# Kernel optimization log

Hardware: AMD Instinct MI355X
Metric: run time of the kernel (lower is better)

## Reference

```python
import jax, jax.numpy as jnp
import numpy as np

D = 768
H = 12
DH = D // H
DFF = 3072
EPS = 1e-5


def setup_inputs() -> dict:
    key = jax.random.key(0)
    ks = jax.random.split(key, 12)
    s = 0.02
    return {
        "x": jax.random.normal(ks[0], (1, 4096, D), jnp.float32),
        "wq": jax.random.normal(ks[1], (D, D), jnp.float32) * s,
        "wk": jax.random.normal(ks[2], (D, D), jnp.float32) * s,
        "wv": jax.random.normal(ks[3], (D, D), jnp.float32) * s,
        "wo": jax.random.normal(ks[4], (D, D), jnp.float32) * s,
        "bo": jnp.zeros((D,), jnp.float32),
        "gamma1": jnp.ones((D,), jnp.float32),
        "beta1": jnp.zeros((D,), jnp.float32),
        "gamma2": jnp.ones((D,), jnp.float32),
        "beta2": jnp.zeros((D,), jnp.float32),
        "w1": jax.random.normal(ks[5], (DFF, D), jnp.float32) * s,
        "b1": jnp.zeros((DFF,), jnp.float32),
        "w2": jax.random.normal(ks[6], (D, DFF), jnp.float32) * s,
        "b2": jnp.zeros((D,), jnp.float32),
    }


def layer_norm(x, gamma, beta):
    mean = jnp.mean(x, axis=-1, keepdims=True)
    var = jnp.mean((x - mean) ** 2, axis=-1, keepdims=True)  # biased variance
    return gamma * (x - mean) / jnp.sqrt(var + EPS) + beta


def reference(x, wq, wk, wv, wo, bo, gamma1, beta1, gamma2, beta2, w1, b1, w2, b2):
    B, T, _ = x.shape
    # --- pre-norm self-attention ---
    h = layer_norm(x, gamma1, beta1)
    q = (h @ wq.T).reshape(B, T, H, DH).transpose(0, 2, 1, 3)  # (B,H,T,dh)
    k = (h @ wk.T).reshape(B, T, H, DH).transpose(0, 2, 1, 3)
    v = (h @ wv.T).reshape(B, T, H, DH).transpose(0, 2, 1, 3)
    scores = jnp.einsum("bhqd,bhkd->bhqk", q, k) / np.sqrt(DH).astype(np.float32)
    probs = jax.nn.softmax(scores, axis=-1)  # dropout = identity (eval)
    attn = jnp.einsum("bhqk,bhkd->bhqd", probs, v)
    attn = attn.transpose(0, 2, 1, 3).reshape(B, T, D)
    x = x + attn @ wo.T + bo
    # --- pre-norm FFN ---
    h2 = layer_norm(x, gamma2, beta2)
    ff = jax.nn.gelu(h2 @ w1.T + b1, approximate=False) @ w2.T + b2
    return x + ff
```

## Files before the change

### kernel.cpp

```cpp
#include <hip/hip_runtime.h>
#include <hip/hip_bf16.h>
#include <math.h>

#define D_MODEL 768
#define NHEAD   12
#define DHEAD   64
#define DFF     3072
#define SEQ     4096

typedef __attribute__((ext_vector_type(8))) short bf16x8;
typedef __attribute__((ext_vector_type(4))) float f32x4;
typedef __attribute__((ext_vector_type(4))) unsigned int u32x4;

__device__ __forceinline__ unsigned short f2bf(float f) {
  union { float f; unsigned int i; } c; c.f = f;
  unsigned int r = c.i + 0x7fffu + ((c.i >> 16) & 1u);
  return (unsigned short)(r >> 16);
}
__device__ __forceinline__ unsigned int pack_bf2(float a, float b) {
  __hip_bfloat162 h = __float22bfloat162_rn(make_float2(a, b));
  return *reinterpret_cast<unsigned int*>(&h);
}
__device__ __forceinline__ float exp2_hw(float x) {
  float r;
  asm("v_exp_f32 %0, %1" : "=v"(r) : "v"(x));
  return r;
}

__global__ void cvt_all(const float* __restrict__ wq, const float* __restrict__ wk,
                        const float* __restrict__ wv, const float* __restrict__ wo,
                        const float* __restrict__ w1, const float* __restrict__ w2,
                        unsigned short* __restrict__ out) {
  const int N4 = 7077888 / 4;
  int i4 = blockIdx.x * blockDim.x + threadIdx.x;
  int stride = gridDim.x * blockDim.x;
  for (; i4 < N4; i4 += stride) {
    int i = i4 * 4;
    const float* src; int j;
    if (i < 2359296) {
      int a = i / 589824; j = i - a * 589824;
      src = a == 0 ? wq : a == 1 ? wk : a == 2 ? wv : wo;
    } else if (i < 4718592) { src = w1; j = i - 2359296; }
    else                    { src = w2; j = i - 4718592; }
    float4 f = *(const float4*)(src + j);
    ushort4 o4;
    o4.x = f2bf(f.x); o4.y = f2bf(f.y); o4.z = f2bf(f.z); o4.w = f2bf(f.w);
    *(ushort4*)(out + i) = o4;
  }
}

__global__ __launch_bounds__(256) void ln_kernel(const float* __restrict__ x,
                                                 const float* __restrict__ gamma,
                                                 const float* __restrict__ beta,
                                                 unsigned short* __restrict__ out) {
  int row = blockIdx.x, tid = threadIdx.x;
  int lane = tid & 63, wv = tid >> 6;
  const float* xr = x + (size_t)row * D_MODEL;
  float v0 = xr[tid], v1 = xr[tid + 256], v2 = xr[tid + 512];
  float s = v0 + v1 + v2;
  __shared__ float red[4];
#pragma unroll
  for (int off = 32; off; off >>= 1) s += __shfl_down(s, off);
  if (lane == 0) red[wv] = s;
  __syncthreads();
  float mean = (red[0] + red[1] + red[2] + red[3]) * (1.0f / D_MODEL);
  __syncthreads();
  float d0 = v0 - mean, d1 = v1 - mean, d2 = v2 - mean;
  float sq = d0 * d0 + d1 * d1 + d2 * d2;
#pragma unroll
  for (int off = 32; off; off >>= 1) sq += __shfl_xor(sq, off);
  if (lane == 0) red[wv] = sq;
  __syncthreads();
  float var = (red[0] + red[1] + red[2] + red[3]) * (1.0f / D_MODEL);
  float rstd = rsqrtf(var + 1e-5f);
  unsigned short* orow = out + (size_t)row * D_MODEL;
  orow[tid]       = f2bf(gamma[tid]       * d0 * rstd + beta[tid]);
  orow[tid + 256] = f2bf(gamma[tid + 256] * d1 * rstd + beta[tid + 256]);
  orow[tid + 512] = f2bf(gamma[tid + 512] * d2 * rstd + beta[tid + 512]);
}

__device__ __forceinline__ void gld_lds(const void* g, void* l) {
  __builtin_amdgcn_global_load_lds((const __attribute__((address_space(1))) unsigned int*)g,
                                   (__attribute__((address_space(3))) unsigned int*)l, 16, 0, 0);
}

template <int MODE, int WM>
__global__ __launch_bounds__(256) void gemm_bt(const unsigned short* __restrict__ A,
                                               const unsigned short* __restrict__ B,
                                               int M, int N, int K,
                                               const float* __restrict__ bias,
                                               const float* __restrict__ residual,
                                               void* __restrict__ out) {
  const int MR = WM / 16;
  const int ASZ = 2 * WM * 32;
  __shared__ __align__(16) unsigned short As[2 * 128 * 32];
  __shared__ __align__(16) unsigned short Bs[2 * 128 * 32];
  const int tid = threadIdx.x;
  const int lane = tid & 63;
  const int wv = tid >> 6;
  const int lo = lane & 15, hi = lane >> 4;
  const int wr = wv >> 1, wc = wv & 1;
  const int row0 = blockIdx.x * (2 * WM), col0 = blockIdx.y * 128;
  const int srow = tid >> 2, scol = (tid & 3) * 8;

  f32x4 zero = {0.f, 0.f, 0.f, 0.f};
  f32x4 acc[MR][4];
#pragma unroll
  for (int m = 0; m < MR; ++m)
#pragma unroll
    for (int n = 0; n < 4; ++n) acc[m][n] = zero;

  const unsigned short* Abase = A + (size_t)(row0 + srow) * K + scol;
  const unsigned short* Bbase = B + (size_t)(col0 + srow) * K + scol;

  auto STAGE = [&](int bi, int kt) {
    unsigned short* Ad = As + bi * ASZ;
    unsigned short* Bd = Bs + bi * 4096;
    gld_lds(Abase + kt, Ad + tid * 8);
    if (WM == 64) gld_lds(Abase + kt + (size_t)64 * K, Ad + 2048 + tid * 8);
    gld_lds(Bbase + kt,                  Bd + tid * 8);
    gld_lds(Bbase + kt + (size_t)64 * K, Bd + 2048 + tid * 8);
  };

  int buf = 0;
  STAGE(0, 0);
  for (int kt = 0; kt < K; kt += 32) {
    __syncthreads();
    if (kt + 32 < K) STAGE(buf ^ 1, kt + 32);
    const unsigned short* Ab = As + buf * ASZ;
    const unsigned short* Bb = Bs + buf * 4096;
    bf16x8 a[MR], b[4];
#pragma unroll
    for (int m = 0; m < MR; ++m)
      a[m] = *(const bf16x8*)(Ab + (wr * WM + m * 16 + lo) * 32 + hi * 8);
#pragma unroll
    for (int n = 0; n < 4; ++n)
      b[n] = *(const bf16x8*)(Bb + (wc * 64 + n * 16 + lo) * 32 + hi * 8);
#pragma unroll
    for (int m = 0; m < MR; ++m)
#pragma unroll
      for (int n = 0; n < 4; ++n)
        acc[m][n] = __builtin_amdgcn_mfma_f32_16x16x32_bf16(a[m], b[n], acc[m][n], 0, 0, 0);
    buf ^= 1;
  }

#pragma unroll
  for (int m = 0; m < MR; ++m) {
#pragma unroll
    for (int n = 0; n < 4; ++n) {
#pragma unroll
      for (int r = 0; r < 4; ++r) {
        int row = row0 + wr * WM + m * 16 + hi * 4 + r;
        int col = col0 + wc * 64 + n * 16 + lo;
        float v = acc[m][n][r];
        if (MODE == 2) {
          ((float*)out)[(size_t)row * N + col] = v + bias[col] + residual[(size_t)row * N + col];
        } else if (MODE == 3) {
          float t = v + bias[col];
          float g = t * __builtin_amdgcn_rcpf(1.0f + __expf(-1.702f * t));
          ((unsigned short*)out)[(size_t)row * N + col] = f2bf(g);
        } else {
          int seg = col / 768;
          int c = col - seg * 768;
          unsigned short* ob = (unsigned short*)out + (size_t)seg * SEQ * D_MODEL;
          float vv = (seg == 0) ? v * 0.18033688011112042f : v;
          if (seg < 2) ob[((size_t)(c >> 6) * M + row) * 64 + (c & 63)] = f2bf(vv);
          else         ob[(size_t)c * M + row] = f2bf(vv);
        }
      }
    }
  }
}

__global__ __launch_bounds__(256, 4) void attn_kernel(const unsigned short* __restrict__ qb,
                                                      const unsigned short* __restrict__ kb,
                                                      const unsigned short* __restrict__ vt,
                                                      unsigned short* __restrict__ outb) {
  __shared__ __align__(16) unsigned short lds[16384 + 128];
  const int tid = threadIdx.x;
  const int lane = tid & 63, wv = tid >> 6;
  const int lo = lane & 15, hi = lane >> 4;
  const int b = blockIdx.x;
  const int u = (b & 7) * 96 + (b >> 3);
  const int head = u >> 6;
  const int q0 = (u & 63) * 64;
  const unsigned short* qh = qb + (size_t)head * SEQ * 64;
  const unsigned short* kh = kb + (size_t)head * SEQ * 64;
  const unsigned short* vh = vt + (size_t)head * 64 * SEQ;

  const int rho  = tid >> 3;
  const int r3   = rho & 7;
  const int krow = (rho & 35) | ((rho & 16) >> 2) | ((rho & 12) << 1);
  const int kofs = krow * 64 + ((tid & 7) ^ r3) * 8;
  const int vcol = ((tid & 7) ^ r3) * 8;
  const int sw   = (lo & 7) << 3;

  f32x4 zero = {0.f, 0.f, 0.f, 0.f};
  bf16x8 qf[2];
#pragma unroll
  for (int kk = 0; kk < 2; ++kk)
    qf[kk] = *(const bf16x8*)(qh + (size_t)(q0 + wv * 16 + lo) * 64 + kk * 32 + hi * 8);

  f32x4 o[4];
  float li = 0.f;
#pragma unroll
  for (int n = 0; n < 4; ++n) o[n] = zero;

  auto STAGE = [&](int bi, int kt) {
    unsigned short* Kd = lds + bi * 4096;
    unsigned short* Vd = lds + 8192 + bi * 4096;
    const unsigned short* kp = kh + (size_t)kt * 64;
    gld_lds(kp + kofs,        Kd + tid * 8);
    gld_lds(kp + 2048 + kofs, Kd + 2048 + tid * 8);
    const unsigned short* vp = vh + kt + vcol;
    gld_lds(vp + (size_t)rho * SEQ,        Vd + tid * 8);
    gld_lds(vp + (size_t)(32 + rho) * SEQ, Vd + 2048 + tid * 8);
  };

  int buf = 0;
  STAGE(0, 0);
  __syncthreads();
  for (int kt = 0; kt < SEQ; kt += 64) {
    if (kt + 64 < SEQ) STAGE(buf ^ 1, kt + 64);
    const unsigned short* Kb = lds + buf * 4096;
    const unsigned short* Vb = lds + 8192 + buf * 4096;
    f32x4 s[4];
    __builtin_amdgcn_s_setprio(1);
#pragma unroll
    for (int n = 0; n < 4; ++n) {
      const int ra = (n * 16 + lo) * 64;
      bf16x8 k0 = *(const bf16x8*)(Kb + ((ra + hi * 8) ^ sw));
      bf16x8 k1 = *(const bf16x8*)(Kb + ((ra + 32 + hi * 8) ^ sw));
      f32x4 t = __builtin_amdgcn_mfma_f32_16x16x32_bf16(k0, qf[0], zero, 0, 0, 0);
      s[n]    = __builtin_amdgcn_mfma_f32_16x16x32_bf16(k1, qf[1], t, 0, 0, 0);
    }
    __builtin_amdgcn_s_setprio(0);
    unsigned int p2[4][2];
#pragma unroll
    for (int n = 0; n < 4; ++n) {
      float e0 = exp2_hw(s[n][0]);
      float e1 = exp2_hw(s[n][1]);
      float e2 = exp2_hw(s[n][2]);
      float e3 = exp2_hw(s[n][3]);
      li += (e0 + e1) + (e2 + e3);
      p2[n][0] = pack_bf2(e0, e1);
      p2[n][1] = pack_bf2(e2, e3);
    }
    __builtin_amdgcn_s_setprio(1);
#pragma unroll
    for (int c = 0; c < 2; ++c) {
      u32x4 pu;
      pu[0] = p2[2 * c][0]; pu[1] = p2[2 * c][1];
      pu[2] = p2[2 * c + 1][0]; pu[3] = p2[2 * c + 1][1];
      bf16x8 pf = *(bf16x8*)&pu;
#pragma unroll
      for (int n = 0; n < 4; ++n) {
        bf16x8 vf = *(const bf16x8*)(Vb + (((n * 16 + lo) * 64 + c * 32 + hi * 8) ^ sw));
        o[n] = __builtin_amdgcn_mfma_f32_16x16x32_bf16(pf, vf, o[n], 0, 0, 0);
      }
    }
    __builtin_amdgcn_s_setprio(0);
    __syncthreads();
    buf ^= 1;
  }

  {
    float t = li;
    t += __shfl_xor(t, 16);
    t += __shfl_xor(t, 32);
    float* pL = (float*)(lds + 16384);
    if (lane < 16) pL[wv * 16 + lane] = 1.0f / t;
  }
  float inv[4];
  {
    float* pL = (float*)(lds + 16384);
#pragma unroll
    for (int r = 0; r < 4; ++r) inv[r] = pL[wv * 16 + hi * 4 + r];
  }

  __syncthreads();
  float* Ow = (float*)lds + wv * 1088;
#pragma unroll
  for (int n = 0; n < 4; ++n)
#pragma unroll
    for (int r = 0; r < 4; ++r)
      Ow[(hi * 4 + r) * 68 + n * 16 + lo] = o[n][r] * inv[r];
  {
    int row = lane >> 2, c0 = (lane & 3) * 16;
    unsigned short tmp[16];
#pragma unroll
    for (int i = 0; i < 16; ++i) tmp[i] = f2bf(Ow[row * 68 + c0 + i]);
    unsigned short* dst = outb + (size_t)(q0 + wv * 16 + row) * D_MODEL + head * 64 + c0;
    *(bf16x8*)dst       = *(const bf16x8*)tmp;
    *(bf16x8*)(dst + 8) = *(const bf16x8*)(tmp + 8);
  }
}

extern "C" void kernel_launch(void* const* d_in, const int* in_sizes, int n_in,
                              void* d_out, int out_size, void* d_ws, size_t ws_size,
                              hipStream_t stream) {
  const float* x      = (const float*)d_in[0];
  const float* wq     = (const float*)d_in[1];
  const float* wk     = (const float*)d_in[2];
  const float* wv     = (const float*)d_in[3];
  const float* wo     = (const float*)d_in[4];
  const float* bo     = (const float*)d_in[5];
  const float* gamma1 = (const float*)d_in[6];
  const float* beta1  = (const float*)d_in[7];
  const float* gamma2 = (const float*)d_in[8];
  const float* beta2  = (const float*)d_in[9];
  const float* w1     = (const float*)d_in[10];
  const float* b1     = (const float*)d_in[11];
  const float* w2     = (const float*)d_in[12];
  const float* b2     = (const float*)d_in[13];
  float* out = (float*)d_out;

  char* ws = (char*)d_ws;
  size_t off = 0;
  auto alloc = [&](size_t bytes) -> void* {
    void* p = ws + off;
    off += (bytes + 255) & ~(size_t)255;
    return p;
  };
  unsigned short* wq_b = (unsigned short*)alloc((size_t)D_MODEL * D_MODEL * 2);
  unsigned short* wk_b = (unsigned short*)alloc((size_t)D_MODEL * D_MODEL * 2);
  unsigned short* wv_b = (unsigned short*)alloc((size_t)D_MODEL * D_MODEL * 2);
  unsigned short* wo_b = (unsigned short*)alloc((size_t)D_MODEL * D_MODEL * 2);
  unsigned short* w1_b = (unsigned short*)alloc((size_t)DFF * D_MODEL * 2);
  unsigned short* w2_b = (unsigned short*)alloc((size_t)D_MODEL * DFF * 2);
  unsigned short* h1   = (unsigned short*)alloc((size_t)SEQ * D_MODEL * 2);
  unsigned short* qh   = (unsigned short*)alloc((size_t)SEQ * D_MODEL * 2);
  unsigned short* kh   = (unsigned short*)alloc((size_t)SEQ * D_MODEL * 2);
  unsigned short* vth  = (unsigned short*)alloc((size_t)SEQ * D_MODEL * 2);
  unsigned short* attnb= (unsigned short*)alloc((size_t)SEQ * D_MODEL * 2);
  float*          x2   = (float*)alloc((size_t)SEQ * D_MODEL * 4);
  unsigned short* h2   = (unsigned short*)alloc((size_t)SEQ * D_MODEL * 2);
  unsigned short* ffb  = (unsigned short*)alloc((size_t)SEQ * DFF * 2);
  (void)ws_size; (void)in_sizes; (void)n_in; (void)out_size;

  cvt_all<<<2048, 256, 0, stream>>>(wq, wk, wv, wo, w1, w2, wq_b);

  ln_kernel<<<SEQ, 256, 0, stream>>>(x, gamma1, beta1, h1);

  dim3 gqkv(SEQ / 128, 2304 / 128);
  gemm_bt<4, 64><<<gqkv, 256, 0, stream>>>(h1, wq_b, SEQ, 2304, D_MODEL, nullptr, nullptr, qh);

  attn_kernel<<<NHEAD * (SEQ / 64), 256, 0, stream>>>(qh, kh, vth, attnb);

  dim3 gwo(SEQ / 64, D_MODEL / 128);
  gemm_bt<2, 32><<<gwo, 256, 0, stream>>>(attnb, wo_b, SEQ, D_MODEL, D_MODEL, bo, x, x2);

  ln_kernel<<<SEQ, 256, 0, stream>>>(x2, gamma2, beta2, h2);

  dim3 gf1(SEQ / 128, DFF / 128);
  gemm_bt<3, 64><<<gf1, 256, 0, stream>>>(h2, w1_b, SEQ, DFF, D_MODEL, b1, nullptr, ffb);

  dim3 gf2(SEQ / 64, D_MODEL / 128);
  gemm_bt<2, 32><<<gf2, 256, 0, stream>>>(ffb, w2_b, SEQ, D_MODEL, DFF, b2, x2, out);
}
```

Measured before the change: 215.2 us.

## Split attention KV range across wave pairs and give each wave two query tiles

Each block's four waves now form two pairs. Each pair processes half of the key/value sequence in its own LDS region, and each wave computes 32 query rows (two M-tiles), so every K/V fragment loaded from LDS feeds two MFMAs. Partial outputs and row sums from the two halves are combined through LDS before normalisation and the bf16 store. The aim is fewer LDS reads per MFMA and a shorter serial KV loop. In exchange, LDS use doubles, launch bounds drop to 2 blocks per CU, and register pressure rises.

```diff
diff --git a/kernel.cpp b/kernel.cpp
--- a/kernel.cpp
+++ b/kernel.cpp
@@ -172,14 +172,16 @@
   }
 }
 
-__global__ __launch_bounds__(256, 4) void attn_kernel(const unsigned short* __restrict__ qb,
+__global__ __launch_bounds__(256, 2) void attn_kernel(const unsigned short* __restrict__ qb,
                                                       const unsigned short* __restrict__ kb,
                                                       const unsigned short* __restrict__ vt,
                                                       unsigned short* __restrict__ outb) {
-  __shared__ __align__(16) unsigned short lds[16384 + 128];
+  __shared__ __align__(16) unsigned short lds[32768];
   const int tid = threadIdx.x;
   const int lane = tid & 63, wv = tid >> 6;
   const int lo = lane & 15, hi = lane >> 4;
+  const int st = wv >> 1;
+  const int qm = wv & 1;
   const int b = blockIdx.x;
   const int u = (b & 7) * 96 + (b >> 3);
   const int head = u >> 6;
@@ -188,75 +190,92 @@
   const unsigned short* kh = kb + (size_t)head * SEQ * 64;
   const unsigned short* vh = vt + (size_t)head * 64 * SEQ;
 
-  const int rho  = tid >> 3;
-  const int r3   = rho & 7;
-  const int krow = (rho & 35) | ((rho & 16) >> 2) | ((rho & 12) << 1);
-  const int kofs = krow * 64 + ((tid & 7) ^ r3) * 8;
-  const int vcol = ((tid & 7) ^ r3) * 8;
-  const int sw   = (lo & 7) << 3;
+  const int ts   = tid >> 7;
+  const int t7   = tid & 127;
+  const int trow = t7 >> 3, tc8 = t7 & 7;
+  const int csw  = (tc8 ^ (trow & 7)) * 8;
+  int kofs[4], vofs[4];
+#pragma unroll
+  for (int o = 0; o < 4; ++o) {
+    int rho = o * 16 + trow;
+    int r5 = rho & 31, half = rho >> 5;
+    int pk = (r5 & 3) | ((r5 & 16) >> 2) | ((r5 & 12) << 1);
+    kofs[o] = (half * 32 + pk) * 64 + csw;
+    vofs[o] = rho * SEQ + csw;
+  }
+  const int sw = (lo & 7) << 3;
 
   f32x4 zero = {0.f, 0.f, 0.f, 0.f};
-  bf16x8 qf[2];
-#pragma unroll
-  for (int kk = 0; kk < 2; ++kk)
-    qf[kk] = *(const bf16x8*)(qh + (size_t)(q0 + wv * 16 + lo) * 64 + kk * 32 + hi * 8);
-
-  f32x4 o[4];
-  float li = 0.f;
-#pragma unroll
-  for (int n = 0; n < 4; ++n) o[n] = zero;
+  bf16x8 qf[2][2];
+#pragma unroll
+  for (int m = 0; m < 2; ++m)
+#pragma unroll
+    for (int kk = 0; kk < 2; ++kk)
+      qf[m][kk] = *(const bf16x8*)(qh + (size_t)(q0 + qm * 32 + m * 16 + lo) * 64 + kk * 32 + hi * 8);
+
+  f32x4 o[2][4];
+  float li[2] = {0.f, 0.f};
+#pragma unroll
+  for (int m = 0; m < 2; ++m)
+#pragma unroll
+    for (int n = 0; n < 4; ++n) o[m][n] = zero;
 
   auto STAGE = [&](int bi, int kt) {
-    unsigned short* Kd = lds + bi * 4096;
-    unsigned short* Vd = lds + 8192 + bi * 4096;
-    const unsigned short* kp = kh + (size_t)kt * 64;
-    gld_lds(kp + kofs,        Kd + tid * 8);
-    gld_lds(kp + 2048 + kofs, Kd + 2048 + tid * 8);
-    const unsigned short* vp = vh + kt + vcol;
-    gld_lds(vp + (size_t)rho * SEQ,        Vd + tid * 8);
-    gld_lds(vp + (size_t)(32 + rho) * SEQ, Vd + 2048 + tid * 8);
+    unsigned short* Kd = lds + ts * 16384 + bi * 4096;
+    unsigned short* Vd = lds + ts * 16384 + 8192 + bi * 4096;
+    const unsigned short* kp = kh + (size_t)(ts * 2048 + kt) * 64;
+    const unsigned short* vp = vh + ts * 2048 + kt;
+#pragma unroll
+    for (int oo = 0; oo < 4; ++oo) {
+      gld_lds(kp + kofs[oo], Kd + oo * 1024 + t7 * 8);
+      gld_lds(vp + vofs[oo], Vd + oo * 1024 + t7 * 8);
+    }
   };
 
+  const unsigned short* base = lds + st * 16384;
   int buf = 0;
   STAGE(0, 0);
   __syncthreads();
-  for (int kt = 0; kt < SEQ; kt += 64) {
-    if (kt + 64 < SEQ) STAGE(buf ^ 1, kt + 64);
-    const unsigned short* Kb = lds + buf * 4096;
-    const unsigned short* Vb = lds + 8192 + buf * 4096;
-    f32x4 s[4];
-    __builtin_amdgcn_s_setprio(1);
+  for (int kt = 0; kt < 2048; kt += 64) {
+    if (kt + 64 < 2048) STAGE(buf ^ 1, kt + 64);
+    const unsigned short* Kb = base + buf * 4096;
+    const unsigned short* Vb = base + 8192 + buf * 4096;
+    unsigned int p2[2][4][2];
 #pragma unroll
     for (int n = 0; n < 4; ++n) {
       const int ra = (n * 16 + lo) * 64;
       bf16x8 k0 = *(const bf16x8*)(Kb + ((ra + hi * 8) ^ sw));
       bf16x8 k1 = *(const bf16x8*)(Kb + ((ra + 32 + hi * 8) ^ sw));
-      f32x4 t = __builtin_amdgcn_mfma_f32_16x16x32_bf16(k0, qf[0], zero, 0, 0, 0);
-      s[n]    = __builtin_amdgcn_mfma_f32_16x16x32_bf16(k1, qf[1], t, 0, 0, 0);
-    }
-    __builtin_amdgcn_s_setprio(0);
-    unsigned int p2[4][2];
-#pragma unroll
-    for (int n = 0; n < 4; ++n) {
-      float e0 = exp2_hw(s[n][0]);
-      float e1 = exp2_hw(s[n][1]);
-      float e2 = exp2_hw(s[n][2]);
-      float e3 = exp2_hw(s[n][3]);
-      li += (e0 + e1) + (e2 + e3);
-      p2[n][0] = pack_bf2(e0, e1);
-      p2[n][1] = pack_bf2(e2, e3);
+#pragma unroll
+      for (int m = 0; m < 2; ++m) {
+        f32x4 t = __builtin_amdgcn_mfma_f32_16x16x32_bf16(k0, qf[m][0], zero, 0, 0, 0);
+        f32x4 sv = __builtin_amdgcn_mfma_f32_16x16x32_bf16(k1, qf[m][1], t, 0, 0, 0);
+        float e0 = exp2_hw(sv[0]);
+        float e1 = exp2_hw(sv[1]);
+        float e2 = exp2_hw(sv[2]);
+        float e3 = exp2_hw(sv[3]);
+        li[m] += (e0 + e1) + (e2 + e3);
+        p2[m][n][0] = pack_bf2(e0, e1);
+        p2[m][n][1] = pack_bf2(e2, e3);
+      }
     }
     __builtin_amdgcn_s_setprio(1);
 #pragma unroll
     for (int c = 0; c < 2; ++c) {
-      u32x4 pu;
-      pu[0] = p2[2 * c][0]; pu[1] = p2[2 * c][1];
-      pu[2] = p2[2 * c + 1][0]; pu[3] = p2[2 * c + 1][1];
-      bf16x8 pf = *(bf16x8*)&pu;
+      bf16x8 pf[2];
+#pragma unroll
+      for (int m = 0; m < 2; ++m) {
+        u32x4 pu;
+        pu[0] = p2[m][2 * c][0]; pu[1] = p2[m][2 * c][1];
+        pu[2] = p2[m][2 * c + 1][0]; pu[3] = p2[m][2 * c + 1][1];
+        pf[m] = *(bf16x8*)&pu;
+      }
 #pragma unroll
       for (int n = 0; n < 4; ++n) {
         bf16x8 vf = *(const bf16x8*)(Vb + (((n * 16 + lo) * 64 + c * 32 + hi * 8) ^ sw));
-        o[n] = __builtin_amdgcn_mfma_f32_16x16x32_bf16(pf, vf, o[n], 0, 0, 0);
+#pragma unroll
+        for (int m = 0; m < 2; ++m)
+          o[m][n] = __builtin_amdgcn_mfma_f32_16x16x32_bf16(pf[m], vf, o[m][n], 0, 0, 0);
       }
     }
     __builtin_amdgcn_s_setprio(0);
@@ -264,33 +283,50 @@
     buf ^= 1;
   }
 
-  {
-    float t = li;
+#pragma unroll
+  for (int m = 0; m < 2; ++m) {
+    float t = li[m];
     t += __shfl_xor(t, 16);
     t += __shfl_xor(t, 32);
-    float* pL = (float*)(lds + 16384);
-    if (lane < 16) pL[wv * 16 + lane] = 1.0f / t;
-  }
-  float inv[4];
+    li[m] = t;
+  }
+  float* Os = (float*)lds;
+  float* Ls = (float*)lds + 4352;
+  if (st == 0) {
+#pragma unroll
+    for (int m = 0; m < 2; ++m)
+#pragma unroll
+      for (int n = 0; n < 4; ++n)
+#pragma unroll
+        for (int r = 0; r < 4; ++r)
+          Os[(qm * 32 + m * 16 + hi * 4 + r) * 68 + n * 16 + lo] = o[m][n][r];
+    if (lane < 16) {
+      Ls[qm * 32 + lane]      = li[0];
+      Ls[qm * 32 + 16 + lane] = li[1];
+    }
+  }
+  __syncthreads();
+  if (st == 1) {
+#pragma unroll
+    for (int m = 0; m < 2; ++m)
+#pragma unroll
+      for (int n = 0; n < 4; ++n)
+#pragma unroll
+        for (int r = 0; r < 4; ++r)
+          Os[(qm * 32 + m * 16 + hi * 4 + r) * 68 + n * 16 + lo] += o[m][n][r];
+    if (lane < 16) {
+      Ls[qm * 32 + lane]      += li[0];
+      Ls[qm * 32 + 16 + lane] += li[1];
+    }
+  }
+  __syncthreads();
   {
-    float* pL = (float*)(lds + 16384);
-#pragma unroll
-    for (int r = 0; r < 4; ++r) inv[r] = pL[wv * 16 + hi * 4 + r];
-  }
-
-  __syncthreads();
-  float* Ow = (float*)lds + wv * 1088;
-#pragma unroll
-  for (int n = 0; n < 4; ++n)
-#pragma unroll
-    for (int r = 0; r < 4; ++r)
-      Ow[(hi * 4 + r) * 68 + n * 16 + lo] = o[n][r] * inv[r];
-  {
-    int row = lane >> 2, c0 = (lane & 3) * 16;
+    int row = tid >> 2, c0 = (tid & 3) * 16;
+    float iv = 1.0f / Ls[row];
     unsigned short tmp[16];
 #pragma unroll
-    for (int i = 0; i < 16; ++i) tmp[i] = f2bf(Ow[row * 68 + c0 + i]);
-    unsigned short* dst = outb + (size_t)(q0 + wv * 16 + row) * D_MODEL + head * 64 + c0;
+    for (int i = 0; i < 16; ++i) tmp[i] = f2bf(Os[row * 68 + c0 + i] * iv);
+    unsigned short* dst = outb + (size_t)(q0 + row) * D_MODEL + head * 64 + c0;
     *(bf16x8*)dst       = *(const bf16x8*)tmp;
     *(bf16x8*)(dst + 8) = *(const bf16x8*)(tmp + 8);
   }
```

Result: slower. 221.6 us (+3.0%).

## Split attention key range across two wave groups per block and merge partials

Applied to the files above, without the earlier changes.

The attention kernel now uses 512 threads per block: two groups of four waves each process half of the key sequence with their own double-buffered LDS region. Partial outputs and softmax denominators are combined through LDS before normalization and the bf16 store. This aims to raise parallelism and latency hiding per query tile, at the cost of double the LDS per block, extra barriers and a reduction step. The merge relies on the softmax having no running max (fixed exp2 scaling), which the existing code already assumes.

```diff
diff --git a/kernel.cpp b/kernel.cpp
--- a/kernel.cpp
+++ b/kernel.cpp
@@ -172,34 +172,38 @@
   }
 }
 
-__global__ __launch_bounds__(256, 4) void attn_kernel(const unsigned short* __restrict__ qb,
+__global__ __launch_bounds__(512, 4) void attn_kernel(const unsigned short* __restrict__ qb,
                                                       const unsigned short* __restrict__ kb,
                                                       const unsigned short* __restrict__ vt,
                                                       unsigned short* __restrict__ outb) {
-  __shared__ __align__(16) unsigned short lds[16384 + 128];
+  __shared__ __align__(16) unsigned short lds[32768];
   const int tid = threadIdx.x;
   const int lane = tid & 63, wv = tid >> 6;
   const int lo = lane & 15, hi = lane >> 4;
+  const int st = wv >> 2;
+  const int qm = wv & 3;
   const int b = blockIdx.x;
   const int u = (b & 7) * 96 + (b >> 3);
   const int head = u >> 6;
   const int q0 = (u & 63) * 64;
   const unsigned short* qh = qb + (size_t)head * SEQ * 64;
-  const unsigned short* kh = kb + (size_t)head * SEQ * 64;
-  const unsigned short* vh = vt + (size_t)head * 64 * SEQ;
-
-  const int rho  = tid >> 3;
+  const unsigned short* kh = kb + (size_t)head * SEQ * 64 + (size_t)st * 2048 * 64;
+  const unsigned short* vh = vt + (size_t)head * 64 * SEQ + st * 2048;
+
+  const int t8   = tid & 255;
+  const int rho  = t8 >> 3;
   const int r3   = rho & 7;
   const int krow = (rho & 35) | ((rho & 16) >> 2) | ((rho & 12) << 1);
-  const int kofs = krow * 64 + ((tid & 7) ^ r3) * 8;
-  const int vcol = ((tid & 7) ^ r3) * 8;
+  const int kofs = krow * 64 + ((t8 & 7) ^ r3) * 8;
+  const int vcol = ((t8 & 7) ^ r3) * 8;
   const int sw   = (lo & 7) << 3;
+  unsigned short* base = lds + st * 16384;
 
   f32x4 zero = {0.f, 0.f, 0.f, 0.f};
   bf16x8 qf[2];
 #pragma unroll
   for (int kk = 0; kk < 2; ++kk)
-    qf[kk] = *(const bf16x8*)(qh + (size_t)(q0 + wv * 16 + lo) * 64 + kk * 32 + hi * 8);
+    qf[kk] = *(const bf16x8*)(qh + (size_t)(q0 + qm * 16 + lo) * 64 + kk * 32 + hi * 8);
 
   f32x4 o[4];
   float li = 0.f;
@@ -207,23 +211,23 @@
   for (int n = 0; n < 4; ++n) o[n] = zero;
 
   auto STAGE = [&](int bi, int kt) {
-    unsigned short* Kd = lds + bi * 4096;
-    unsigned short* Vd = lds + 8192 + bi * 4096;
+    unsigned short* Kd = base + bi * 4096;
+    unsigned short* Vd = base + 8192 + bi * 4096;
     const unsigned short* kp = kh + (size_t)kt * 64;
-    gld_lds(kp + kofs,        Kd + tid * 8);
-    gld_lds(kp + 2048 + kofs, Kd + 2048 + tid * 8);
+    gld_lds(kp + kofs,        Kd + t8 * 8);
+    gld_lds(kp + 2048 + kofs, Kd + 2048 + t8 * 8);
     const unsigned short* vp = vh + kt + vcol;
-    gld_lds(vp + (size_t)rho * SEQ,        Vd + tid * 8);
-    gld_lds(vp + (size_t)(32 + rho) * SEQ, Vd + 2048 + tid * 8);
+    gld_lds(vp + (size_t)rho * SEQ,        Vd + t8 * 8);
+    gld_lds(vp + (size_t)(32 + rho) * SEQ, Vd + 2048 + t8 * 8);
   };
 
   int buf = 0;
   STAGE(0, 0);
   __syncthreads();
-  for (int kt = 0; kt < SEQ; kt += 64) {
-    if (kt + 64 < SEQ) STAGE(buf ^ 1, kt + 64);
-    const unsigned short* Kb = lds + buf * 4096;
-    const unsigned short* Vb = lds + 8192 + buf * 4096;
+  for (int kt = 0; kt < 2048; kt += 64) {
+    if (kt + 64 < 2048) STAGE(buf ^ 1, kt + 64);
+    const unsigned short* Kb = base + buf * 4096;
+    const unsigned short* Vb = base + 8192 + buf * 4096;
     f32x4 s[4];
     __builtin_amdgcn_s_setprio(1);
 #pragma unroll
@@ -268,31 +272,36 @@
     float t = li;
     t += __shfl_xor(t, 16);
     t += __shfl_xor(t, 32);
-    float* pL = (float*)(lds + 16384);
-    if (lane < 16) pL[wv * 16 + lane] = 1.0f / t;
-  }
-  float inv[4];
+    li = t;
+  }
+  __syncthreads();
+  float* Os = (float*)lds;
+  float* Ls = (float*)lds + 4352;
+  if (lane < 16) Ls[st * 64 + qm * 16 + lane] = li;
+  if (st == 0) {
+#pragma unroll
+    for (int n = 0; n < 4; ++n)
+#pragma unroll
+      for (int r = 0; r < 4; ++r)
+        Os[(qm * 16 + hi * 4 + r) * 68 + n * 16 + lo] = o[n][r];
+  }
+  __syncthreads();
+  if (st == 1) {
+#pragma unroll
+    for (int n = 0; n < 4; ++n)
+#pragma unroll
+      for (int r = 0; r < 4; ++r)
+        Os[(qm * 16 + hi * 4 + r) * 68 + n * 16 + lo] += o[n][r];
+  }
+  __syncthreads();
   {
-    float* pL = (float*)(lds + 16384);
-#pragma unroll
-    for (int r = 0; r < 4; ++r) inv[r] = pL[wv * 16 + hi * 4 + r];
-  }
-
-  __syncthreads();
-  float* Ow = (float*)lds + wv * 1088;
-#pragma unroll
-  for (int n = 0; n < 4; ++n)
-#pragma unroll
-    for (int r = 0; r < 4; ++r)
-      Ow[(hi * 4 + r) * 68 + n * 16 + lo] = o[n][r] * inv[r];
-  {
-    int row = lane >> 2, c0 = (lane & 3) * 16;
-    unsigned short tmp[16];
-#pragma unroll
-    for (int i = 0; i < 16; ++i) tmp[i] = f2bf(Ow[row * 68 + c0 + i]);
-    unsigned short* dst = outb + (size_t)(q0 + wv * 16 + row) * D_MODEL + head * 64 + c0;
-    *(bf16x8*)dst       = *(const bf16x8*)tmp;
-    *(bf16x8*)(dst + 8) = *(const bf16x8*)(tmp + 8);
+    int row = tid >> 3, c0 = (tid & 7) * 8;
+    float iv = 1.0f / (Ls[row] + Ls[64 + row]);
+    unsigned short tmp[8];
+#pragma unroll
+    for (int i = 0; i < 8; ++i) tmp[i] = f2bf(Os[row * 68 + c0 + i] * iv);
+    unsigned short* dst = outb + (size_t)(q0 + row) * D_MODEL + head * 64 + c0;
+    *(bf16x8*)dst = *(const bf16x8*)tmp;
   }
 }
 
@@ -345,7 +354,7 @@
   dim3 gqkv(SEQ / 128, 2304 / 128);
   gemm_bt<4, 64><<<gqkv, 256, 0, stream>>>(h1, wq_b, SEQ, 2304, D_MODEL, nullptr, nullptr, qh);
 
-  attn_kernel<<<NHEAD * (SEQ / 64), 256, 0, stream>>>(qh, kh, vth, attnb);
+  attn_kernel<<<NHEAD * (SEQ / 64), 512, 0, stream>>>(qh, kh, vth, attnb);
 
   dim3 gwo(SEQ / 64, D_MODEL / 128);
   gemm_bt<2, 32><<<gwo, 256, 0, stream>>>(attnb, wo_b, SEQ, D_MODEL, D_MODEL, bo, x, x2);
```

Result: no change. 216.3 us (+0.5%).
